# Kernel tuning notes

Hardware: AMD Instinct MI355X
Metric: run time of the kernel (lower is better)

The kernel has to match this reference:

```python
import jax, jax.numpy as jnp
import numpy as np

B, T, C = 4, 2048, 1024
NQ, D = 8, C // 8  # n_query heads, head dim = n_embd // 8


def setup_inputs() -> dict:
    key = jax.random.key(0)
    ks = jax.random.split(key, 6)
    s = 0.02
    return {
        "x": jax.random.normal(ks[0], (B, T, C), dtype=jnp.float32),
        "Wk": jax.random.normal(ks[1], (C, D), dtype=jnp.float32) * s,
        "Wv": jax.random.normal(ks[2], (C, D), dtype=jnp.float32) * s,
        "Wq": jax.random.normal(ks[3], (NQ, C, D), dtype=jnp.float32) * s,
        "Wp": jax.random.normal(ks[4], (NQ * D, C), dtype=jnp.float32) * s,
        "bp": jnp.zeros((C,), dtype=jnp.float32),
    }


def reference(x, Wk, Wv, Wq, Wp, bp):
    b, t, c = x.shape
    scale = c ** -0.5  # original scales by n_embd**-0.5, not head-dim
    k = x @ Wk                                   # [B,T,D] shared across heads (MQA)
    v = x @ Wv                                   # [B,T,D]
    q = jnp.einsum("btc,qcd->bqtd", x, Wq)       # [B,NQ,T,D]
    wei = jnp.einsum("bqtd,bsd->bqts", q, k) * scale
    causal = jnp.tril(jnp.ones((t, t), dtype=bool))
    wei = jnp.where(causal, wei, -jnp.inf)
    wei = jax.nn.softmax(wei, axis=-1)
    out = jnp.einsum("bqts,bsd->btqd", wei, v)   # [B,T,NQ,D]
    out = out.reshape(b, t, -1)                  # concat heads -> [B,T,NQ*D]
    return out @ Wp + bp
```

## Files before the change

kernel.cpp:

```cpp
#include <hip/hip_runtime.h>
#include <hip/hip_bf16.h>
#include <cstddef>
#include <cstdint>

#define B 4
#define T 2048
#define C 1024
#define NQ 8
#define D 128
#define M_ROWS (B * T)
#define NTOT (2 * D + NQ * D)

typedef __bf16 bf16x8 __attribute__((ext_vector_type(8)));
typedef float  f32x4  __attribute__((ext_vector_type(4)));

__device__ __forceinline__ ushort f2bf(float f) {
    union { float f; uint32_t u; } v; v.f = f;
    const uint32_t r = (v.u + 0x7fffu + ((v.u >> 16) & 1u)) >> 16;
    return (ushort)r;
}

__device__ __forceinline__ void gld_lds16(const ushort* g, ushort* lds_uniform) {
    __builtin_amdgcn_global_load_lds(
        (const __attribute__((address_space(1))) void*)g,
        (__attribute__((address_space(3))) void*)lds_uniform, 16, 0, 0);
}

__global__ __launch_bounds__(256) void xcvt(const float* __restrict__ x,
                                            ushort* __restrict__ xb) {
    const size_t i = ((size_t)blockIdx.x * 256 + threadIdx.x) * 8;
    const float4 a = *(const float4*)(x + i);
    const float4 b = *(const float4*)(x + i + 4);
    uint4 o;
    o.x = f2bf(a.x) | ((uint32_t)f2bf(a.y) << 16);
    o.y = f2bf(a.z) | ((uint32_t)f2bf(a.w) << 16);
    o.z = f2bf(b.x) | ((uint32_t)f2bf(b.y) << 16);
    o.w = f2bf(b.z) | ((uint32_t)f2bf(b.w) << 16);
    *(uint4*)(xb + i) = o;
}

__device__ __forceinline__ void wtrans_body(const float* __restrict__ src,
                                            ushort* __restrict__ dst, int NC,
                                            int bx, int by) {
    __shared__ ushort Ts[64][72];
    const int tid = threadIdx.x;
    const int k0 = by * 64, c0 = bx * 64;
    {
        const int r = tid >> 2, cq = tid & 3;
#pragma unroll
        for (int i = 0; i < 4; ++i) {
            const int cc = cq * 16 + i * 4;
            const float4 v = *(const float4*)(src + (size_t)(k0 + r) * NC + c0 + cc);
            uint2 o;
            o.x = f2bf(v.x) | ((uint32_t)f2bf(v.y) << 16);
            o.y = f2bf(v.z) | ((uint32_t)f2bf(v.w) << 16);
            *(uint2*)(&Ts[r][cc]) = o;
        }
    }
    __syncthreads();
    {
        const int n = tid >> 2, kq = tid & 3;
        ushort vv[16];
#pragma unroll
        for (int j = 0; j < 16; ++j) vv[j] = Ts[kq * 16 + j][n];
        uint4 o0, o1;
        o0.x = vv[0] | ((uint32_t)vv[1] << 16);  o0.y = vv[2] | ((uint32_t)vv[3] << 16);
        o0.z = vv[4] | ((uint32_t)vv[5] << 16);  o0.w = vv[6] | ((uint32_t)vv[7] << 16);
        o1.x = vv[8] | ((uint32_t)vv[9] << 16);  o1.y = vv[10] | ((uint32_t)vv[11] << 16);
        o1.z = vv[12] | ((uint32_t)vv[13] << 16); o1.w = vv[14] | ((uint32_t)vv[15] << 16);
        ushort* d = dst + (size_t)(c0 + n) * C + k0 + kq * 16;
        *(uint4*)d = o0;
        *(uint4*)(d + 8) = o1;
    }
}

__global__ __launch_bounds__(256) void wtrans_qkv(const float* __restrict__ Wk,
                                                  const float* __restrict__ Wv,
                                                  const float* __restrict__ Wq,
                                                  ushort* __restrict__ WcatT) {
    const int z = blockIdx.z;
    const float* src;
    int rbase;
    if (z == 0)      { src = Wk; rbase = 0; }
    else if (z == 1) { src = Wv; rbase = D; }
    else             { src = Wq + (size_t)(z - 2) * C * D; rbase = 2 * D + (z - 2) * D; }
    wtrans_body(src, WcatT + (size_t)rbase * C, D, blockIdx.x, blockIdx.y);
}

__global__ __launch_bounds__(256) void wtrans_p(const float* __restrict__ Wp,
                                                ushort* __restrict__ WpT) {
    wtrans_body(Wp, WpT, C, blockIdx.x, blockIdx.y);
}

__global__ __launch_bounds__(256) void vtrans(const ushort* __restrict__ qkv,
                                              ushort* __restrict__ vbT) {
    __shared__ ushort Ts[64][136];
    const int tid = threadIdx.x;
    const int kb0 = blockIdx.x * 64;
    {
        const int r = tid >> 2, cq = tid & 3;
        const ushort* src = qkv + (size_t)(kb0 + r) * NTOT + D;
#pragma unroll
        for (int i = 0; i < 4; ++i) {
            const int cc = (cq * 4 + i) * 8;
            *(uint4*)(&Ts[r][cc]) = *(const uint4*)(src + cc);
        }
    }
    __syncthreads();
    {
        const int d = tid >> 1, half = tid & 1;
        ushort vv[32];
#pragma unroll
        for (int k = 0; k < 32; ++k) vv[k] = Ts[half * 32 + k][d];
        uint32_t dw[16];
#pragma unroll
        for (int i = 0; i < 16; ++i) dw[i] = vv[i] | ((uint32_t)vv[16 + i] << 16);
        uint32_t* dst = (uint32_t*)(vbT + (size_t)d * M_ROWS + kb0 + half * 32);
#pragma unroll
        for (int i = 0; i < 4; ++i)
            *(uint4*)(dst + i * 4) = *(uint4*)(&dw[i * 4]);
    }
}

template <bool BF16_OUT>
__global__ __launch_bounds__(256) void gemm_mfma(const ushort* __restrict__ A,
                                                 const ushort* __restrict__ Bt,
                                                 void* __restrict__ Cout,
                                                 const float* __restrict__ bias,
                                                 const int Nout) {
    __shared__ ushort As[128 * 32];
    __shared__ ushort Bs[128 * 32];
    const int tid  = threadIdx.x;
    const int lane = tid & 63;
    const int w    = tid >> 6;
    const int col  = lane & 15;
    const int quad = lane >> 4;
    const int row0 = blockIdx.y * 128;
    const int col0 = blockIdx.x * 128;
    const int wm = w & 1, wn = w >> 1;

    const int srow = lane >> 2;
    const int skk  = (lane & 3) * 8;

    f32x4 acc[4][4];
#pragma unroll
    for (int i = 0; i < 4; ++i)
#pragma unroll
        for (int j = 0; j < 4; ++j) acc[i][j] = (f32x4){0.f, 0.f, 0.f, 0.f};

    for (int k0 = 0; k0 < C; k0 += 32) {
        __syncthreads();
#pragma unroll
        for (int j = 0; j < 2; ++j) {
            const int ci = w * 2 + j;
            const int r  = ci * 16 + srow;
            gld_lds16(A  + (size_t)(row0 + r) * C + k0 + skk, &As[ci * 512]);
            gld_lds16(Bt + (size_t)(col0 + r) * C + k0 + skk, &Bs[ci * 512]);
        }
        __syncthreads();

        bf16x8 af[4], bfr[4];
#pragma unroll
        for (int i = 0; i < 4; ++i)
            af[i] = *(const bf16x8*)&As[(wm * 64 + i * 16 + col) * 32 + quad * 8];
#pragma unroll
        for (int j = 0; j < 4; ++j)
            bfr[j] = *(const bf16x8*)&Bs[(wn * 64 + j * 16 + col) * 32 + quad * 8];
#pragma unroll
        for (int i = 0; i < 4; ++i)
#pragma unroll
            for (int j = 0; j < 4; ++j)
                acc[i][j] = __builtin_amdgcn_mfma_f32_16x16x32_bf16(af[i], bfr[j], acc[i][j], 0, 0, 0);
    }

#pragma unroll
    for (int i = 0; i < 4; ++i) {
#pragma unroll
        for (int r = 0; r < 4; ++r) {
            const int grow = row0 + wm * 64 + i * 16 + quad * 4 + r;
#pragma unroll
            for (int j = 0; j < 4; ++j) {
                const int gcol = col0 + wn * 64 + j * 16 + col;
                const float v = acc[i][j][r];
                if (BF16_OUT) {
                    ((ushort*)Cout)[(size_t)grow * Nout + gcol] = f2bf(v);
                } else {
                    ((float*)Cout)[(size_t)grow * Nout + gcol] = v + bias[gcol];
                }
            }
        }
    }
}

__global__ __launch_bounds__(256) void attn_mfma(const ushort* __restrict__ qkv,
                                                 const ushort* __restrict__ vbT,
                                                 ushort* __restrict__ attb) {
    __shared__ ushort Ks4[4][64][32];
    __shared__ ushort Vt4[4][128][16];
    __shared__ ushort Pt[4][2][16][32];

    const int tid  = threadIdx.x;
    const int lane = tid & 63;
    const int w    = tid >> 6;
    const int col  = lane & 15;
    const int quad = lane >> 4;
    const int h    = blockIdx.y;
    const int b    = blockIdx.z;
    const int qb_i = (b & 1) ? (gridDim.x - 1 - blockIdx.x) : blockIdx.x;
    const int q0   = qb_i * 64;
    const int myq  = q0 + w * 16 + col;

    const ushort* qrow = qkv + (size_t)(b * T + myq) * NTOT + 2 * D + h * D;
    bf16x8 qf[4];
#pragma unroll
    for (int kb2 = 0; kb2 < 4; ++kb2)
        qf[kb2] = *(const bf16x8*)(qrow + kb2 * 32 + quad * 8);

    const ushort* kbase = qkv + (size_t)b * T * NTOT;
    const ushort* vbase = vbT + (size_t)b * T;

    f32x4 O[8];
#pragma unroll
    for (int i = 0; i < 8; ++i) O[i] = (f32x4){0.f, 0.f, 0.f, 0.f};
    float l_r[4] = {0.f, 0.f, 0.f, 0.f};

    const int ntiles = qb_i + 1;
    const int sk_key = lane >> 2;
    const int sk_d   = (lane & 3) * 8;
    const int sv_half = (lane & 1) * 8;

    for (int it = 0; it < ntiles; ++it) {
        const int s0 = it * 64;
        __syncthreads();
#pragma unroll
        for (int kg = 0; kg < 4; ++kg) {
            gld_lds16(kbase + (size_t)(s0 + kg * 16 + sk_key) * NTOT + w * 32 + sk_d,
                      &Ks4[w][kg * 16][0]);
        }
#pragma unroll
        for (int i2 = 0; i2 < 4; ++i2) {
            const int d = (i2 * 64 + lane) >> 1;
            gld_lds16(vbase + (size_t)d * M_ROWS + s0 + w * 16 + sv_half,
                      &Vt4[w][i2 * 32][0]);
        }
        __syncthreads();

        f32x4 S[4];
#pragma unroll
        for (int sub = 0; sub < 4; ++sub) {
            f32x4 a = (f32x4){0.f, 0.f, 0.f, 0.f};
#pragma unroll
            for (int kb2 = 0; kb2 < 4; ++kb2) {
                bf16x8 kf = *(const bf16x8*)(&Ks4[kb2][sub * 16 + col][quad * 8]);
                a = __builtin_amdgcn_mfma_f32_16x16x32_bf16(qf[kb2], kf, a, 0, 0, 0);
            }
            S[sub] = a;
        }

#pragma unroll
        for (int r = 0; r < 4; ++r) {
            const int qq = q0 + w * 16 + quad * 4 + r;
            float p[4];
#pragma unroll
            for (int sub = 0; sub < 4; ++sub) {
                const int key = s0 + sub * 16 + col;
                const float s = (key > qq) ? -1e30f : S[sub][r] * 0.03125f;
                p[sub] = __expf(s);
            }
            l_r[r] += (p[0] + p[1]) + (p[2] + p[3]);
            *(uint32_t*)(&Pt[w][0][quad * 4 + r][col * 2]) =
                f2bf(p[0]) | ((uint32_t)f2bf(p[1]) << 16);
            *(uint32_t*)(&Pt[w][1][quad * 4 + r][col * 2]) =
                f2bf(p[2]) | ((uint32_t)f2bf(p[3]) << 16);
        }

        bf16x8 pa0 = *(const bf16x8*)(&Pt[w][0][col][quad * 8]);
        bf16x8 pa1 = *(const bf16x8*)(&Pt[w][1][col][quad * 8]);
        const int kg0 = quad >> 1;
        const int ko  = (quad & 1) * 8;
#pragma unroll
        for (int nt = 0; nt < 8; ++nt) {
            bf16x8 vf0 = *(const bf16x8*)(&Vt4[kg0][nt * 16 + col][ko]);
            bf16x8 vf1 = *(const bf16x8*)(&Vt4[2 + kg0][nt * 16 + col][ko]);
            O[nt] = __builtin_amdgcn_mfma_f32_16x16x32_bf16(pa0, vf0, O[nt], 0, 0, 0);
            O[nt] = __builtin_amdgcn_mfma_f32_16x16x32_bf16(pa1, vf1, O[nt], 0, 0, 0);
        }
    }

#pragma unroll
    for (int r = 0; r < 4; ++r) {
        float s = l_r[r];
#pragma unroll
        for (int off = 1; off < 16; off <<= 1) s += __shfl_xor(s, off);
        const float inv = 1.0f / s;
        const int t = q0 + w * 16 + quad * 4 + r;
        ushort* orow = attb + (size_t)(b * T + t) * C + h * D;
#pragma unroll
        for (int nt = 0; nt < 8; ++nt) orow[nt * 16 + col] = f2bf(O[nt][r] * inv);
    }
}

extern "C" void kernel_launch(void* const* d_in, const int* in_sizes, int n_in,
                              void* d_out, int out_size, void* d_ws, size_t ws_size,
                              hipStream_t stream) {
    const float* x  = (const float*)d_in[0];
    const float* Wk = (const float*)d_in[1];
    const float* Wv = (const float*)d_in[2];
    const float* Wq = (const float*)d_in[3];
    const float* Wp = (const float*)d_in[4];
    const float* bp = (const float*)d_in[5];
    float* out = (float*)d_out;

    char* ws = (char*)d_ws;
    ushort* xb    = (ushort*)ws;
    ushort* attb  = xb;
    ushort* qkv   = (ushort*)(ws + (size_t)16  * 1024 * 1024);
    ushort* WcatT = (ushort*)(ws + (size_t)36  * 1024 * 1024);
    ushort* WpT   = (ushort*)(ws + (size_t)39  * 1024 * 1024);
    ushort* vbT   = (ushort*)(ws + (size_t)41  * 1024 * 1024);

    xcvt<<<(size_t)M_ROWS * C / (256 * 8), 256, 0, stream>>>(x, xb);
    wtrans_qkv<<<dim3(D / 64, C / 64, 2 + NQ), 256, 0, stream>>>(Wk, Wv, Wq, WcatT);
    wtrans_p<<<dim3(C / 64, C / 64), 256, 0, stream>>>(Wp, WpT);

    gemm_mfma<true><<<dim3(NTOT / 128, M_ROWS / 128), 256, 0, stream>>>(
        xb, WcatT, qkv, nullptr, NTOT);

    vtrans<<<M_ROWS / 64, 256, 0, stream>>>(qkv, vbT);

    attn_mfma<<<dim3(T / 64, NQ, B), 256, 0, stream>>>(qkv, vbT, attb);

    gemm_mfma<false><<<dim3(C / 128, M_ROWS / 128), 256, 0, stream>>>(
        attb, WpT, out, bp, C);
}
```

Measured before the change: 249.9 us.

## Register-prefetch next K/V tile in attention and merge weight transpose kernels

The attention loop now loads the next K and V tile from global memory into registers while the MFMA work for the current tile runs, then writes them to LDS between two barriers. This replaces the direct global-to-LDS loads that were issued and waited on before each tile's compute, and is meant to hide load latency. The two weight-transpose kernels are merged into a single launch to save one kernel launch. The trade is extra register pressure, which could lower occupancy, and two barriers per iteration remain.

```diff
diff --git a/kernel.cpp b/kernel.cpp
--- a/kernel.cpp
+++ b/kernel.cpp
@@ -74,22 +74,25 @@
     }
 }
 
-__global__ __launch_bounds__(256) void wtrans_qkv(const float* __restrict__ Wk,
+__global__ __launch_bounds__(256) void wtrans_all(const float* __restrict__ Wk,
                                                   const float* __restrict__ Wv,
                                                   const float* __restrict__ Wq,
-                                                  ushort* __restrict__ WcatT) {
-    const int z = blockIdx.z;
-    const float* src;
-    int rbase;
-    if (z == 0)      { src = Wk; rbase = 0; }
-    else if (z == 1) { src = Wv; rbase = D; }
-    else             { src = Wq + (size_t)(z - 2) * C * D; rbase = 2 * D + (z - 2) * D; }
-    wtrans_body(src, WcatT + (size_t)rbase * C, D, blockIdx.x, blockIdx.y);
-}
-
-__global__ __launch_bounds__(256) void wtrans_p(const float* __restrict__ Wp,
-                                                ushort* __restrict__ WpT) {
-    wtrans_body(Wp, WpT, C, blockIdx.x, blockIdx.y);
+                                                  const float* __restrict__ Wp,
+                                                  ushort* __restrict__ WcatT,
+                                                  ushort* __restrict__ WpT) {
+    const int id = blockIdx.x;
+    if (id < 320) {
+        const int z = id >> 5, rem = id & 31;
+        const float* src;
+        int rbase;
+        if (z == 0)      { src = Wk; rbase = 0; }
+        else if (z == 1) { src = Wv; rbase = D; }
+        else             { src = Wq + (size_t)(z - 2) * C * D; rbase = 2 * D + (z - 2) * D; }
+        wtrans_body(src, WcatT + (size_t)rbase * C, D, rem & 1, rem >> 1);
+    } else {
+        const int id2 = id - 320;
+        wtrans_body(Wp, WpT, C, id2 & 15, id2 >> 4);
+    }
 }
 
 __global__ __launch_bounds__(256) void vtrans(const ushort* __restrict__ qkv,
@@ -229,21 +232,34 @@
     const int sk_d   = (lane & 3) * 8;
     const int sv_half = (lane & 1) * 8;
 
+    uint4 kpre[4], vpre[4];
+    auto load_tile = [&](int s0) {
+#pragma unroll
+        for (int kg = 0; kg < 4; ++kg)
+            kpre[kg] = *(const uint4*)(kbase + (size_t)(s0 + kg * 16 + sk_key) * NTOT + w * 32 + sk_d);
+#pragma unroll
+        for (int i2 = 0; i2 < 4; ++i2) {
+            const int d = (i2 * 64 + lane) >> 1;
+            vpre[i2] = *(const uint4*)(vbase + (size_t)d * M_ROWS + s0 + w * 16 + sv_half);
+        }
+    };
+    auto store_tile = [&]() {
+#pragma unroll
+        for (int kg = 0; kg < 4; ++kg)
+            *(uint4*)(&Ks4[w][kg * 16][0] + (size_t)lane * 8) = kpre[kg];
+#pragma unroll
+        for (int i2 = 0; i2 < 4; ++i2)
+            *(uint4*)(&Vt4[w][i2 * 32][0] + (size_t)lane * 8) = vpre[i2];
+    };
+
+    load_tile(0);
+    store_tile();
+    __syncthreads();
+
     for (int it = 0; it < ntiles; ++it) {
         const int s0 = it * 64;
-        __syncthreads();
-#pragma unroll
-        for (int kg = 0; kg < 4; ++kg) {
-            gld_lds16(kbase + (size_t)(s0 + kg * 16 + sk_key) * NTOT + w * 32 + sk_d,
-                      &Ks4[w][kg * 16][0]);
-        }
-#pragma unroll
-        for (int i2 = 0; i2 < 4; ++i2) {
-            const int d = (i2 * 64 + lane) >> 1;
-            gld_lds16(vbase + (size_t)d * M_ROWS + s0 + w * 16 + sv_half,
-                      &Vt4[w][i2 * 32][0]);
-        }
-        __syncthreads();
+        const bool more = (it + 1 < ntiles);
+        if (more) load_tile(s0 + 64);
 
         f32x4 S[4];
 #pragma unroll
@@ -285,6 +301,12 @@
             O[nt] = __builtin_amdgcn_mfma_f32_16x16x32_bf16(pa0, vf0, O[nt], 0, 0, 0);
             O[nt] = __builtin_amdgcn_mfma_f32_16x16x32_bf16(pa1, vf1, O[nt], 0, 0, 0);
         }
+
+        if (more) {
+            __syncthreads();
+            store_tile();
+            __syncthreads();
+        }
     }
 
 #pragma unroll
@@ -320,8 +342,7 @@
     ushort* vbT   = (ushort*)(ws + (size_t)41  * 1024 * 1024);
 
     xcvt<<<(size_t)M_ROWS * C / (256 * 8), 256, 0, stream>>>(x, xb);
-    wtrans_qkv<<<dim3(D / 64, C / 64, 2 + NQ), 256, 0, stream>>>(Wk, Wv, Wq, WcatT);
-    wtrans_p<<<dim3(C / 64, C / 64), 256, 0, stream>>>(Wp, WpT);
+    wtrans_all<<<576, 256, 0, stream>>>(Wk, Wv, Wq, Wp, WcatT, WpT);
 
     gemm_mfma<true><<<dim3(NTOT / 128, M_ROWS / 128), 256, 0, stream>>>(
         xb, WcatT, qkv, nullptr, NTOT);
```

Result: slower. 389.5 us (+55.8%).
